# Performance work log

Hardware: AMD Instinct MI355X
Metric: run time of the kernel (lower is better)

## Reference

```python
import jax, jax.numpy as jnp
import numpy as np

# NTU RGB+D 25-joint skeleton edges (1-based)
NTU_EDGES = [(1,2),(2,21),(3,21),(4,3),(5,21),(6,5),(7,6),(8,7),(9,21),(10,9),
             (11,10),(12,11),(13,1),(14,13),(15,14),(16,15),(17,1),(18,17),
             (19,18),(20,19),(22,23),(23,8),(24,25),(25,12)]
NUM_SCALES = 13
NUM_POINT = 25


def build_A_powers(num_scales=NUM_SCALES, v=NUM_POINT):
    # MS-G3D disentangled multi-scale aggregation: exact-k-hop adjacencies, each
    # with self loops, symmetrically normalized, stacked along dim 0 -> (K*V, V).
    A = np.zeros((v, v))
    for i, j in NTU_EDGES:
        A[i - 1, j - 1] = 1.0
        A[j - 1, i - 1] = 1.0
    I = np.eye(v)
    mats = []
    for k in range(num_scales):
        if k == 0:
            Ak = I.copy()
        else:
            Ak = np.minimum(np.linalg.matrix_power(A + I, k), 1) \
               - np.minimum(np.linalg.matrix_power(A + I, k - 1), 1)
            Ak = Ak + I  # with_self=True
        d = Ak.sum(-1)
        dinv = np.where(d > 0, d ** -0.5, 0.0)
        mats.append((dinv[:, None] * Ak) * dinv[None, :])
    return np.concatenate(mats, 0).astype(np.float32)


def batchnorm(x, g, b, axes, ch_axis, eps=1e-5):
    # torch BatchNorm in training mode: biased batch stats + affine
    mean = jnp.mean(x, axes, keepdims=True)
    var = jnp.mean((x - mean) ** 2, axes, keepdims=True)
    shape = [1] * x.ndim
    shape[ch_axis] = -1
    return (x - mean) * jax.lax.rsqrt(var + eps) * g.reshape(shape) + b.reshape(shape)


def ms_gcn(x, A_powers, A_res, W, b, g, beta, num_scales):
    # x: (N, C, T, V); A: (K*V, V)
    A = A_powers + A_res
    support = jnp.einsum('vu,nctu->nctv', A, x)            # (N, C, T, K*V)
    N, C, T, KV = support.shape
    V = KV // num_scales
    support = support.reshape(N, C, T, num_scales, V).transpose(0, 3, 1, 2, 4)
    support = support.reshape(N, num_scales * C, T, V)     # (N, K*C, T, V)
    out = jnp.einsum('oc,nctv->notv', W, support) + b[None, :, None, None]  # 1x1 conv
    out = batchnorm(out, g, beta, (0, 2, 3), 1)
    return jax.nn.relu(out)


def lstm(x, Wih, Whh, bih, bhh):
    # single-layer batch_first LSTM, zero initial state; torch gate order i,f,g,o
    B = x.shape[0]
    H = Whh.shape[1]
    xp = jnp.einsum('bsd,hd->bsh', x, Wih) + bih + bhh     # precompute input proj

    def step(carry, xt):
        h, c = carry
        gates = xt + h @ Whh.T
        i, f, g, o = jnp.split(gates, 4, axis=-1)
        c = jax.nn.sigmoid(f) * c + jax.nn.sigmoid(i) * jnp.tanh(g)
        h = jax.nn.sigmoid(o) * jnp.tanh(c)
        return (h, c), h

    init = (jnp.zeros((B, H), x.dtype), jnp.zeros((B, H), x.dtype))
    _, ys = jax.lax.scan(step, init, jnp.swapaxes(xp, 0, 1))
    return jnp.swapaxes(ys, 0, 1)                          # (B, S, H)


def logsig_rnn(x, n_segments, Wih, Whh, bih, bhh):
    # x: (B, T, d). Depth-2 log-signature per time segment + segment start point,
    # concatenated and fed to an LSTM (Logsig-RNN layer).
    B, T, d = x.shape
    t_vec = np.array([int(round(float(v))) for v in np.linspace(1, T, n_segments + 1)])
    starts = t_vec[:-1] - 1
    ends = t_vec[1:] - 1
    L = int((ends - starts).max()) + 1
    # pad segments to fixed length by repeating the last point (zero increments)
    idx = np.minimum(starts[:, None] + np.arange(L)[None, :], ends[:, None])  # (S, L)
    pts = x[:, idx, :]                                     # (B, S, L, d)
    rel = pts - pts[:, :, :1, :]
    inc = rel[:, :, -1, :]                                 # level-1: total increment
    dx = pts[:, :, 1:, :] - pts[:, :, :-1, :]
    Mm = jnp.einsum('bsli,bslj->bsij', rel[:, :, :-1, :], dx)
    iu, ju = np.triu_indices(d, k=1)
    levy = 0.5 * (Mm[:, :, iu, ju] - Mm[:, :, ju, iu])     # level-2 (Lyndon basis)
    feats = jnp.concatenate([x[:, starts, :], inc, levy], axis=-1)
    return lstm(feats, Wih, Whh, bih, bhh)


def setup_inputs() -> dict:
    key = jax.random.key(0)
    ks = iter(jax.random.split(key, 16))
    N, C, T, V, M = 2, 3, 100, 25, 2
    c1, c2, num_class, K = 96, 192, 60, NUM_SCALES

    def randn(shape, scale):
        return jax.random.normal(next(ks), shape, jnp.float32) * scale

    ls1 = c1 + c1 * (c1 - 1) // 2     # 4656
    ls2 = c2 + c2 * (c2 - 1) // 2     # 18528
    in1 = c1 + ls1                    # 4752
    in2 = c2 + ls2                    # 18720
    Ap = jnp.asarray(build_A_powers())
    return {
        'x': jax.random.normal(next(ks), (N, C, T, V, M), jnp.float32),
        'length': jax.random.randint(next(ks), (N,), 0, T),
        'data_bn_g': jnp.ones((M * V * C,)), 'data_bn_b': jnp.zeros((M * V * C,)),
        'A_powers1': Ap,
        'A_res1': jax.random.uniform(next(ks), Ap.shape, jnp.float32, -1e-6, 1e-6),
        'W1': randn((c1, K * C), (K * C) ** -0.5), 'b1': jnp.zeros((c1,)),
        'bn1_g': jnp.ones((c1,)), 'bn1_b': jnp.zeros((c1,)),
        'Wih1': randn((4 * c1, in1), in1 ** -0.5), 'Whh1': randn((4 * c1, c1), c1 ** -0.5),
        'bih1': jnp.zeros((4 * c1,)), 'bhh1': jnp.zeros((4 * c1,)),
        'bnseg1_g': jnp.ones((50,)), 'bnseg1_b': jnp.zeros((50,)),
        'A_powers2': Ap,
        'A_res2': jax.random.uniform(next(ks), Ap.shape, jnp.float32, -1e-6, 1e-6),
        'W2': randn((c2, K * c1), (K * c1) ** -0.5), 'b2': jnp.zeros((c2,)),
        'bn2_g': jnp.ones((c2,)), 'bn2_b': jnp.zeros((c2,)),
        'Wih2': randn((4 * c2, in2), in2 ** -0.5), 'Whh2': randn((4 * c2, c2), c2 ** -0.5),
        'bih2': jnp.zeros((4 * c2,)), 'bhh2': jnp.zeros((4 * c2,)),
        'bnseg2_g': jnp.ones((30,)), 'bnseg2_b': jnp.zeros((30,)),
        'fcW': randn((num_class, c2), c2 ** -0.5), 'fcb': jnp.zeros((num_class,)),
    }


def reference(x, length, data_bn_g, data_bn_b, A_powers1, A_res1, W1, b1, bn1_g, bn1_b,
              Wih1, Whh1, bih1, bhh1, bnseg1_g, bnseg1_b, A_powers2, A_res2, W2, b2,
              bn2_g, bn2_b, Wih2, Whh2, bih2, bhh2, bnseg2_g, bnseg2_b, fcW, fcb):
    # `length` is accepted but unused, as in the original forward.
    N, C, T, V, M = x.shape
    K = A_powers1.shape[0] // V
    c1, c2 = W1.shape[0], W2.shape[0]
    S1, S2 = 50, 30

    h = x.transpose(0, 4, 3, 1, 2).reshape(N, M * V * C, T)
    h = batchnorm(h, data_bn_g, data_bn_b, (0, 2), 1)
    h = h.reshape(N * M, V, C, T).transpose(0, 2, 3, 1)            # (NM, C, T, V)

    h = jax.nn.relu(ms_gcn(h, A_powers1, A_res1, W1, b1, bn1_g, bn1_b, K))
    h = h.transpose(0, 3, 2, 1).reshape(N * M * V, T, c1)
    h = logsig_rnn(h, S1, Wih1, Whh1, bih1, bhh1)                  # (NMV, S1, c1)
    h = batchnorm(h, bnseg1_g, bnseg1_b, (0, 2), 1)
    h = h.reshape(N * M, V, S1, c1).transpose(0, 3, 2, 1)          # (NM, c1, S1, V)

    h = jax.nn.relu(ms_gcn(h, A_powers2, A_res2, W2, b2, bn2_g, bn2_b, K))
    h = h.transpose(0, 3, 2, 1).reshape(N * M * V, S1, c2)
    h = logsig_rnn(h, S2, Wih2, Whh2, bih2, bhh2)                  # (NMV, S2, c2)
    h = batchnorm(h, bnseg2_g, bnseg2_b, (0, 2), 1)
    h = h.reshape(N * M, V, S2, c2).transpose(0, 3, 2, 1)          # (NM, c2, S2, V)

    pooled = h.reshape(N, M, c2, -1).mean(axis=3).mean(axis=1)     # (N, c2)
    return pooled @ fcW.T + fcb
```

## Files before the change

### kernel.cpp

```cpp
#include <hip/hip_runtime.h>
#include <cmath>
#include <cstdint>
#include <cstddef>

typedef unsigned short bf16_t;
typedef __attribute__((ext_vector_type(8))) short short8;
typedef __attribute__((ext_vector_type(4))) float floatx4;
typedef __attribute__((ext_vector_type(2))) _Float16 half2_t;

__device__ __forceinline__ float bf2f(bf16_t b){
  unsigned int u = ((unsigned int)b) << 16;
  return __uint_as_float(u);
}
__device__ __forceinline__ bf16_t f2bf(float f){
  unsigned int u = __float_as_uint(f);
  unsigned int r = (u + 0x7fffu + ((u >> 16) & 1u)) >> 16;
  return (bf16_t)r;
}
__device__ __forceinline__ unsigned int f2bf2(float a, float b){
  return (unsigned int)f2bf(a) | ((unsigned int)f2bf(b) << 16);
}
__device__ __forceinline__ float sigf(float x){ return 1.0f / (1.0f + expf(-x)); }

__device__ __forceinline__ float dot2(half2_t a, half2_t b, float c){
#if __has_builtin(__builtin_amdgcn_fdot2)
  return __builtin_amdgcn_fdot2(a, b, c, false);
#else
  return c + (float)a.x * (float)b.x + (float)a.y * (float)b.y;
#endif
}

__device__ __forceinline__ void gload_lds16(const bf16_t* g, bf16_t* lds){
  __builtin_amdgcn_global_load_lds(
      (const __attribute__((address_space(1))) unsigned int*)g,
      (__attribute__((address_space(3))) unsigned int*)lds, 16, 0, 0);
}

__global__ void prep_misc(const float* __restrict__ a1, const float* __restrict__ r1, float* __restrict__ o1,
                          const float* __restrict__ a2, const float* __restrict__ r2, float* __restrict__ o2,
                          const float* __restrict__ bi1, const float* __restrict__ bh1, float* __restrict__ ob1,
                          const float* __restrict__ bi2, const float* __restrict__ bh2, float* __restrict__ ob2,
                          const float* __restrict__ Whh1, half2_t* __restrict__ Wp1,
                          const float* __restrict__ Whh2, half2_t* __restrict__ Wp2,
                          unsigned short* __restrict__ lut1, unsigned short* __restrict__ lut2,
                          float* __restrict__ stats, bf16_t* __restrict__ A2mat){
  int i = blockIdx.x * blockDim.x + threadIdx.x;
  if (i < 8125){ o1[i] = a1[i] + r1[i]; o2[i] = a2[i] + r2[i]; }
  if (i < 384) ob1[i] = bi1[i] + bh1[i];
  if (i < 768) ob2[i] = bi2[i] + bh2[i];
  if (i < 736) stats[i] = 0.f;
  if (i < 18432){
    int t = i % 384, j2 = i / 384;
    half2_t w; w.x = (_Float16)Whh1[(size_t)t * 96 + 2 * j2];
    w.y = (_Float16)Whh1[(size_t)t * 96 + 2 * j2 + 1];
    Wp1[i] = w;
  }
  if (i < 73728){
    int t = i % 768, j2 = i / 768;
    half2_t w; w.x = (_Float16)Whh2[(size_t)t * 192 + 2 * j2];
    w.y = (_Float16)Whh2[(size_t)t * 192 + 2 * j2 + 1];
    Wp2[i] = w;
  }
  if (i < 4560){
    int d = 96, p = i;
    int r = (int)(((2.0 * d - 1.0) - sqrt((2.0 * d - 1.0) * (2.0 * d - 1.0) - 8.0 * (double)p)) * 0.5);
    if (r < 0) r = 0;
    while (r + 1 <= d - 2 && (r + 1) * (d - 1) - ((r + 1) * r) / 2 <= p) ++r;
    while (r > 0 && r * (d - 1) - (r * (r - 1)) / 2 > p) --r;
    int jj = p - (r * (d - 1) - (r * (r - 1)) / 2);
    lut1[p] = (unsigned short)((r << 8) | (r + 1 + jj));
  }
  if (i < 18336){
    int d = 192, p = i;
    int r = (int)(((2.0 * d - 1.0) - sqrt((2.0 * d - 1.0) * (2.0 * d - 1.0) - 8.0 * (double)p)) * 0.5);
    if (r < 0) r = 0;
    while (r + 1 <= d - 2 && (r + 1) * (d - 1) - ((r + 1) * r) / 2 <= p) ++r;
    while (r > 0 && r * (d - 1) - (r * (r - 1)) / 2 > p) --r;
    int jj = p - (r * (d - 1) - (r * (r - 1)) / 2);
    lut2[p] = (unsigned short)((r << 8) | (r + 1 + jj));
  }
  if (i < 160000){
    int row = i >> 5, col = 1248 + (i & 31);
    A2mat[(size_t)row * 1280 + col] = 0;
  }
}

__global__ void f2bf_pad8(const float* __restrict__ in, bf16_t* __restrict__ out,
                          int R, int Kin, int Kout){
  int idx = blockIdx.x * blockDim.x + threadIdx.x;
  int ko8 = Kout >> 3;
  if (idx >= R * ko8) return;
  int r = idx / ko8, k8 = (idx % ko8) << 3;
  uint4 u;
  if (k8 + 8 <= Kin){
    const float4* p = reinterpret_cast<const float4*>(in + (size_t)r * Kin + k8);
    float4 x0 = p[0], x1 = p[1];
    u.x = f2bf2(x0.x, x0.y); u.y = f2bf2(x0.z, x0.w);
    u.z = f2bf2(x1.x, x1.y); u.w = f2bf2(x1.z, x1.w);
  } else {
    u.x = u.y = u.z = u.w = 0u;
  }
  *reinterpret_cast<uint4*>(out + (size_t)r * Kout + k8) = u;
}

__global__ void data_bn_kernel(const float* __restrict__ x, const float* __restrict__ g,
                               const float* __restrict__ bb, float* __restrict__ h1,
                               int N, int C, int T, int V, int M){
  int ch = blockIdx.x;
  int m = ch / (V * C);
  int v = (ch / C) % V;
  int c = ch % C;
  int tid = threadIdx.x;
  int cnt = N * T;
  float s = 0.f, s2 = 0.f;
  for (int i = tid; i < cnt; i += 64){
    int n = i / T, t = i % T;
    float val = x[(((size_t)(n * C + c) * T + t) * V + v) * M + m];
    s += val; s2 += val * val;
  }
  for (int off = 32; off; off >>= 1){ s += __shfl_down(s, off); s2 += __shfl_down(s2, off); }
  s = __shfl(s, 0); s2 = __shfl(s2, 0);
  float mean = s / cnt;
  float rstd = rsqrtf(s2 / cnt - mean * mean + 1e-5f);
  float gg = g[ch], bo = bb[ch];
  for (int i = tid; i < cnt; i += 64){
    int n = i / T, t = i % T;
    float val = x[(((size_t)(n * C + c) * T + t) * V + v) * M + m];
    float y = (val - mean) * rstd * gg + bo;
    h1[((size_t)((n * M + m) * C + c) * T + t) * V + v] = y;
  }
}

__global__ void support1_kernel(const float* __restrict__ A, const float* __restrict__ hin,
                                float* __restrict__ sup, int total){
  int idx = blockIdx.x * blockDim.x + threadIdx.x;
  if (idx >= total) return;
  int w = idx % 325;
  int rest = idx / 325;
  const float* row = hin + (size_t)rest * 25;
  const float* ar = A + w * 25;
  float acc = 0.f;
  #pragma unroll
  for (int u = 0; u < 25; ++u) acc += ar[u] * row[u];
  sup[idx] = acc;
}

__global__ void gcn1_out_kernel(const float* __restrict__ sup, const float* __restrict__ W1,
                                const float* __restrict__ b1, float* __restrict__ y1, int NM, int T){
  int idx = blockIdx.x * blockDim.x + threadIdx.x;
  int total = NM * T * 25 * 96;
  if (idx >= total) return;
  int o = idx % 96;
  int v = (idx / 96) % 25;
  int t = (idx / (96 * 25)) % T;
  int nm = idx / (96 * 25 * T);
  float acc = b1[o];
  #pragma unroll
  for (int k = 0; k < 13; ++k)
    #pragma unroll
    for (int c = 0; c < 3; ++c)
      acc += W1[o * 39 + k * 3 + c] * sup[(size_t)((nm * 3 + c) * T + t) * 325 + k * 25 + v];
  y1[idx] = acc;
}

__global__ void colstats_atomic(const float* __restrict__ mat, int R,
                                float* __restrict__ sum, float* __restrict__ sumsq){
  int col = threadIdx.x;
  int Cc = blockDim.x;
  float s = 0.f, s2 = 0.f;
  for (int r = blockIdx.x; r < R; r += gridDim.x){
    float v = mat[(size_t)r * Cc + col];
    s += v; s2 += v * v;
  }
  atomicAdd(&sum[col], s);
  atomicAdd(&sumsq[col], s2);
}

__global__ void segstats_atomic(const float* __restrict__ lout, int R2, int S,
                                float* __restrict__ sum, float* __restrict__ sumsq){
  int t = threadIdx.x;
  int H = blockDim.x;
  int nw = H >> 6;
  __shared__ float ra[4], rb[4];
  int lane = t & 63, wid = t >> 6;
  for (int r = blockIdx.x; r < R2; r += gridDim.x){
    int s = r % S;
    float v = lout[(size_t)r * H + t];
    float a = v, b2 = v * v;
    for (int off = 32; off; off >>= 1){ a += __shfl_down(a, off); b2 += __shfl_down(b2, off); }
    if (lane == 0){ ra[wid] = a; rb[wid] = b2; }
    __syncthreads();
    if (t == 0){
      float sa = 0.f, sb = 0.f;
      for (int w = 0; w < nw; ++w){ sa += ra[w]; sb += rb[w]; }
      atomicAdd(&sum[s], sa);
      atomicAdd(&sumsq[s], sb);
    }
    __syncthreads();
  }
}

__global__ void bn_relu_seq_kernel(const float* __restrict__ ymat, const float* __restrict__ sum,
                                   const float* __restrict__ sumsq, const float* __restrict__ g,
                                   const float* __restrict__ bb, float* __restrict__ xseq,
                                   int NM, int T, int H, int R){
  int idx = blockIdx.x * blockDim.x + threadIdx.x;
  int total = NM * T * 25 * H;
  if (idx >= total) return;
  int o = idx % H;
  int v = (idx / H) % 25;
  int t = (idx / (H * 25)) % T;
  int nm = idx / (H * 25 * T);
  float mean = sum[o] / R;
  float rstd = rsqrtf(sumsq[o] / R - mean * mean + 1e-5f);
  float val = (ymat[idx] - mean) * rstd * g[o] + bb[o];
  val = fmaxf(val, 0.f);
  int b = nm * 25 + v;
  xseq[((size_t)b * T + t) * H + o] = val;
}

struct SegTable { int st[50]; int en[50]; };

__global__ void feats_kernel(const float* __restrict__ xseq, bf16_t* __restrict__ feats,
                             SegTable segs, const unsigned short* __restrict__ lut,
                             int T, int d, int S, int L, int pairs, int rowlenP){
  __shared__ float pts[4][192];
  int bs = blockIdx.x;
  int b = bs / S, s = bs % S;
  int st = segs.st[s], en = segs.en[s];
  int nt = blockDim.x, tid = threadIdx.x;
  for (int l = 0; l < L; ++l){
    int t = st + l; if (t > en) t = en;
    for (int i = tid; i < d; i += nt) pts[l][i] = xseq[((size_t)b * T + t) * d + i];
  }
  __syncthreads();
  int rowlen = 2 * d + pairs;
  bf16_t* frow = feats + (size_t)bs * rowlenP;
  for (int i = tid; i < d; i += nt){
    frow[i] = f2bf(pts[0][i]);
    frow[d + i] = f2bf(pts[L - 1][i] - pts[0][i]);
  }
  for (int i = tid + rowlen; i < rowlenP; i += nt) frow[i] = 0;
  int Lm2 = L - 2;
  bf16_t* lrow = frow + 2 * d;
  for (int p = tid; p < pairs; p += nt){
    int e = lut[p];
    int i = e >> 8, j = e & 255;
    float acc = 0.f;
    for (int l = 1; l <= Lm2; ++l){
      float ri = pts[l][i] - pts[0][i], rj = pts[l][j] - pts[0][j];
      float di = pts[l + 1][i] - pts[l][i], dj = pts[l + 1][j] - pts[l][j];
      acc += ri * dj - rj * di;
    }
    lrow[p] = f2bf(0.5f * acc);
  }
}

__global__ __launch_bounds__(256)
void gemm_mfma_nt_split(const bf16_t* __restrict__ A, const bf16_t* __restrict__ B,
                        float* __restrict__ P, int M, int N, int K){
  __shared__ bf16_t As[128 * 64];
  __shared__ bf16_t Bs[128 * 64];
  const int tid = threadIdx.x;
  const int lane = tid & 63, wv = tid >> 6;
  const int bm = blockIdx.x * 128, bn = blockIdx.y * 128;
  const int wr = (wv >> 1) * 64, wc = (wv & 1) * 64;
  const int m_l = lane & 15, q = lane >> 4;

  const int ksteps = K >> 6;
  const int Z = gridDim.z, z = blockIdx.z;
  const int per = (ksteps + Z - 1) / Z;
  const int ks0 = z * per;
  const int ks1 = (ks0 + per < ksteps) ? ks0 + per : ksteps;

  const int rlane = lane >> 3;
  const int slane = lane & 7;
  const int colc = (slane ^ rlane) * 8;
  const bf16_t* gA[4]; const bf16_t* gB[4];
  bf16_t* lA[4]; bf16_t* lB[4];
  #pragma unroll
  for (int it = 0; it < 4; ++it){
    int c = it * 4 + wv;
    int rowA = bm + c * 8 + rlane; if (rowA > M - 1) rowA = M - 1;
    int rowB = bn + c * 8 + rlane; if (rowB > N - 1) rowB = N - 1;
    gA[it] = A + (size_t)rowA * K + colc;
    gB[it] = B + (size_t)rowB * K + colc;
    lA[it] = &As[c * 512];
    lB[it] = &Bs[c * 512];
  }
  const int sxor = m_l & 7;

  floatx4 acc[4][4] = {};
  for (int ks = ks0; ks < ks1; ++ks){
    int k0 = ks << 6;
    __syncthreads();
    #pragma unroll
    for (int it = 0; it < 4; ++it){
      gload_lds16(gA[it] + k0, lA[it]);
      gload_lds16(gB[it] + k0, lB[it]);
    }
    __syncthreads();
    #pragma unroll
    for (int half = 0; half < 2; ++half){
      const int scol = ((half * 4 + q) ^ sxor) * 8;
      short8 af[4], bfr[4];
      #pragma unroll
      for (int i = 0; i < 4; ++i){
        af[i]  = *reinterpret_cast<const short8*>(&As[(wr + i * 16 + m_l) * 64 + scol]);
        bfr[i] = *reinterpret_cast<const short8*>(&Bs[(wc + i * 16 + m_l) * 64 + scol]);
      }
      #pragma unroll
      for (int mi = 0; mi < 4; ++mi)
        #pragma unroll
        for (int ni = 0; ni < 4; ++ni)
          acc[mi][ni] = __builtin_amdgcn_mfma_f32_16x16x32_bf16(af[mi], bfr[ni], acc[mi][ni], 0, 0, 0);
    }
  }

  float* Pz = P + (size_t)z * M * N;
  #pragma unroll
  for (int mi = 0; mi < 4; ++mi){
    int row0 = bm + wr + mi * 16 + q * 4;
    #pragma unroll
    for (int r = 0; r < 4; ++r){
      int row = row0 + r;
      if (row < M){
        #pragma unroll
        for (int ni = 0; ni < 4; ++ni){
          int col = bn + wc + ni * 16 + m_l;
          if (col < N) Pz[(size_t)row * N + col] = acc[mi][ni][r];
        }
      }
    }
  }
}

__global__ void reduce_split_bias(const float* __restrict__ P, const float* __restrict__ bias,
                                  float* __restrict__ out, int MN, int N, int Z){
  int i4 = (blockIdx.x * blockDim.x + threadIdx.x) * 4;
  if (i4 >= MN) return;
  const float4 bv = *reinterpret_cast<const float4*>(bias + (i4 % N));
  float4 s = bv;
  for (int z = 0; z < Z; ++z){
    const float4 p = *reinterpret_cast<const float4*>(P + (size_t)z * MN + i4);
    s.x += p.x; s.y += p.y; s.z += p.z; s.w += p.w;
  }
  *reinterpret_cast<float4*>(out + i4) = s;
}

template <int H2C, int BLK, int Z>
__global__ __launch_bounds__(BLK)
void lstm_kernel(const float* __restrict__ P, const float* __restrict__ bias,
                 const half2_t* __restrict__ Wp, float* __restrict__ out,
                 int S, int MN){
  constexpr int H = 2 * H2C;
  constexpr int H4 = 4 * H;
  __shared__ _Float16 __attribute__((aligned(16))) hsh[H];
  __shared__ float gv[H4];
  const int b = blockIdx.x, t = threadIdx.x;
  half2_t w[H2C];
  const half2_t* wp = Wp + t;
  #pragma unroll
  for (int j2 = 0; j2 < H2C; ++j2) w[j2] = wp[(size_t)j2 * H4];
  float cc = 0.f;
  if (t < H) hsh[t] = (_Float16)0.f;
  const float bval = bias[t];
  __syncthreads();
  const half2_t* hp = reinterpret_cast<const half2_t*>(hsh);
  for (int s = 0; s < S; ++s){
    size_t rowoff = ((size_t)b * S + s) * H4 + t;
    float pv[Z];
    #pragma unroll
    for (int z = 0; z < Z; ++z) pv[z] = P[(size_t)z * MN + rowoff];
    float a0 = bval, a1 = 0.f, a2 = 0.f, a3 = 0.f;
    #pragma unroll
    for (int z = 0; z < Z; ++z) a0 += pv[z];
    #pragma unroll
    for (int j2 = 0; j2 < H2C; j2 += 4){
      a0 = dot2(w[j2],     hp[j2],     a0);
      a1 = dot2(w[j2 + 1], hp[j2 + 1], a1);
      a2 = dot2(w[j2 + 2], hp[j2 + 2], a2);
      a3 = dot2(w[j2 + 3], hp[j2 + 3], a3);
    }
    gv[t] = (a0 + a1) + (a2 + a3);
    __syncthreads();
    if (t < H){
      float ig = sigf(gv[t]);
      float fg = sigf(gv[H + t]);
      float gg = tanhf(gv[2 * H + t]);
      float og = sigf(gv[3 * H + t]);
      cc = fg * cc + ig * gg;
      float hh = og * tanhf(cc);
      hsh[t] = (_Float16)hh;
      out[((size_t)b * S + s) * H + t] = hh;
    }
    __syncthreads();
  }
}

__global__ void bnseg_to_g2in_kernel(const float* __restrict__ lout, const float* __restrict__ sum,
                                     const float* __restrict__ sumsq, const float* __restrict__ g,
                                     const float* __restrict__ bb, float* __restrict__ g2in,
                                     int B, int S, int H, int cnt){
  int idx = blockIdx.x * blockDim.x + threadIdx.x;
  int total = B * S * H;
  if (idx >= total) return;
  int hh = idx % H;
  int s = (idx / H) % S;
  int b = idx / (H * S);
  float mean = sum[s] / cnt;
  float rstd = rsqrtf(sumsq[s] / cnt - mean * mean + 1e-5f);
  float val = (lout[idx] - mean) * rstd * g[s] + bb[s];
  int nm = b / 25, v = b % 25;
  g2in[((size_t)((nm * H + hh) * S) + s) * 25 + v] = val;
}

__global__ void support2_kernel(const float* __restrict__ A, const float* __restrict__ g2in,
                                bf16_t* __restrict__ A2mat, int NM, int C1, int S){
  int idx = blockIdx.x * blockDim.x + threadIdx.x;
  int total = NM * C1 * S * 325;
  if (idx >= total) return;
  int w = idx % 325;
  int s = (idx / 325) % S;
  int c = (idx / (325 * S)) % C1;
  int nm = idx / (325 * S * C1);
  const float* row = g2in + ((size_t)((nm * C1 + c) * S) + s) * 25;
  const float* ar = A + w * 25;
  float acc = 0.f;
  #pragma unroll
  for (int u = 0; u < 25; ++u) acc += ar[u] * row[u];
  int k = w / 25, v = w % 25;
  A2mat[((size_t)((nm * S + s) * 25 + v)) * 1280 + k * C1 + c] = f2bf(acc);
}

__global__ void pool_kernel(const float* __restrict__ lout2, const float* __restrict__ sum,
                            const float* __restrict__ sumsq, const float* __restrict__ g,
                            const float* __restrict__ bb, float* __restrict__ pooled,
                            int S, int H, int scnt){
  int n = blockIdx.x / H;
  int o = blockIdx.x % H;
  float acc = 0.f;
  int cnt = 2 * 25 * S;
  for (int i = threadIdx.x; i < cnt; i += 64){
    int m = i / (25 * S);
    int r = i % (25 * S);
    int v = r / S;
    int s = r % S;
    int b = (n * 2 + m) * 25 + v;
    float val = lout2[((size_t)b * S + s) * H + o];
    float mean = sum[s] / scnt;
    float rstd = rsqrtf(sumsq[s] / scnt - mean * mean + 1e-5f);
    val = (val - mean) * rstd * g[s] + bb[s];
    acc += val;
  }
  for (int off = 32; off; off >>= 1) acc += __shfl_down(acc, off);
  if (threadIdx.x == 0) pooled[n * H + o] = acc / cnt;
}

__global__ void fc_kernel(const float* __restrict__ pooled, const float* __restrict__ fcW,
                          const float* __restrict__ fcb, float* __restrict__ outp){
  int idx = blockIdx.x * blockDim.x + threadIdx.x;
  if (idx >= 120) return;
  int n = idx / 60, cls = idx % 60;
  float acc = fcb[cls];
  for (int o = 0; o < 192; ++o) acc += pooled[n * 192 + o] * fcW[cls * 192 + o];
  outp[idx] = acc;
}

static void make_segs(int T, int S, SegTable& tab, int& L){
  double step = (double)(T - 1) / (double)S;
  long long tv[51];
  for (int i = 0; i <= S; ++i){
    double v = 1.0 + step * (double)i;
    tv[i] = llrint(v);
  }
  L = 0;
  for (int s = 0; s < S; ++s){
    tab.st[s] = (int)tv[s] - 1;
    tab.en[s] = (int)tv[s + 1] - 1;
    int len = tab.en[s] - tab.st[s] + 1;
    if (len > L) L = len;
  }
  for (int s = S; s < 50; ++s){ tab.st[s] = 0; tab.en[s] = 0; }
  if (L > 4) L = 4;
}

extern "C" void kernel_launch(void* const* d_in, const int* in_sizes, int n_in,
                              void* d_out, int out_size, void* d_ws, size_t ws_size,
                              hipStream_t stream){
  const float* x         = (const float*)d_in[0];
  const float* data_bn_g = (const float*)d_in[2];
  const float* data_bn_b = (const float*)d_in[3];
  const float* A_powers1 = (const float*)d_in[4];
  const float* A_res1    = (const float*)d_in[5];
  const float* W1        = (const float*)d_in[6];
  const float* b1        = (const float*)d_in[7];
  const float* bn1_g     = (const float*)d_in[8];
  const float* bn1_b     = (const float*)d_in[9];
  const float* Wih1      = (const float*)d_in[10];
  const float* Whh1      = (const float*)d_in[11];
  const float* bih1      = (const float*)d_in[12];
  const float* bhh1      = (const float*)d_in[13];
  const float* bnseg1_g  = (const float*)d_in[14];
  const float* bnseg1_b  = (const float*)d_in[15];
  const float* A_powers2 = (const float*)d_in[16];
  const float* A_res2    = (const float*)d_in[17];
  const float* W2        = (const float*)d_in[18];
  const float* b2        = (const float*)d_in[19];
  const float* bn2_g     = (const float*)d_in[20];
  const float* bn2_b     = (const float*)d_in[21];
  const float* Wih2      = (const float*)d_in[22];
  const float* Whh2      = (const float*)d_in[23];
  const float* bih2      = (const float*)d_in[24];
  const float* bhh2      = (const float*)d_in[25];
  const float* bnseg2_g  = (const float*)d_in[26];
  const float* bnseg2_b  = (const float*)d_in[27];
  const float* fcW       = (const float*)d_in[28];
  const float* fcb       = (const float*)d_in[29];
  float* out = (float*)d_out;

  const int N = 2, C = 3, T = 100, V = 25, M = 2, NM = 4;
  const int K = 13, C1 = 96, C2 = 192;
  const int S1 = 50, S2 = 30;
  const int B = 100;
  const int IN1 = 4752, IN2 = 18720;
  const int IN1P = 4800, IN2P = 18752;
  const int P1 = 4560, P2 = 18336;
  const int KG2 = 1248, KG2P = 1280;
  const int Z1 = 5, Z2 = 6, ZG = 4;

  size_t off = 0;
  char* base = (char*)d_ws;
  auto alloc = [&](size_t nbytes) -> void* {
    off = (off + 255) & ~(size_t)255;
    void* p = base + off;
    off += nbytes;
    return p;
  };
  float* A1full = (float*)alloc(325 * 25 * 4);
  float* A2full = (float*)alloc(325 * 25 * 4);
  float* h1     = (float*)alloc((size_t)NM * C * T * V * 4);
  float* sup1   = (float*)alloc((size_t)NM * C * T * 325 * 4);
  float* y1mat  = (float*)alloc((size_t)NM * T * V * C1 * 4);
  float* stats  = (float*)alloc(736 * 4);
  float* st1a = stats, *st1b = stats + 96;
  float* sg1a = stats + 192, *sg1b = stats + 242;
  float* st2a = stats + 292, *st2b = stats + 484;
  float* sg2a = stats + 676, *sg2b = stats + 706;
  float* xseq1  = (float*)alloc((size_t)B * T * C1 * 4);
  float* l1out  = (float*)alloc((size_t)B * S1 * C1 * 4);
  float* g2in   = (float*)alloc((size_t)NM * C1 * S1 * V * 4);
  bf16_t* A2mat = (bf16_t*)alloc((size_t)NM * S1 * V * KG2P * 2);
  float* y2mat  = (float*)alloc((size_t)NM * S1 * V * C2 * 4);
  float* xseq2  = (float*)alloc((size_t)B * S1 * C2 * 4);
  float* l2out  = (float*)alloc((size_t)B * S2 * C2 * 4);
  float* pooled = (float*)alloc(2 * C2 * 4);
  float* bias1  = (float*)alloc(4 * C1 * 4);
  float* bias2  = (float*)alloc(4 * C2 * 4);
  half2_t* Wp1  = (half2_t*)alloc((size_t)(C1 / 2) * 4 * C1 * 4);
  half2_t* Wp2  = (half2_t*)alloc((size_t)(C2 / 2) * 4 * C2 * 4);
  bf16_t* Wih1b = (bf16_t*)alloc((size_t)4 * C1 * IN1P * 2);
  bf16_t* Wih2b = (bf16_t*)alloc((size_t)4 * C2 * IN2P * 2);
  bf16_t* W2b   = (bf16_t*)alloc((size_t)C2 * KG2P * 2);
  unsigned short* lut1 = (unsigned short*)alloc((size_t)P1 * 2);
  unsigned short* lut2 = (unsigned short*)alloc((size_t)P2 * 2);
  size_t pmax = (size_t)Z2 * 3000 * 768;
  {
    size_t p1s = (size_t)Z1 * 5000 * 384; if (p1s > pmax) pmax = p1s;
    size_t pgs = (size_t)ZG * 5000 * 192; if (pgs > pmax) pmax = pgs;
  }
  float* Pbuf = (float*)alloc(pmax * 4);
  bf16_t* feats = (bf16_t*)alloc((size_t)B * S2 * IN2P * 2);
  (void)ws_size; (void)in_sizes; (void)n_in; (void)out_size;

  prep_misc<<<625, 256, 0, stream>>>(A_powers1, A_res1, A1full, A_powers2, A_res2, A2full,
                                     bih1, bhh1, bias1, bih2, bhh2, bias2,
                                     Whh1, Wp1, Whh2, Wp2, lut1, lut2, stats, A2mat);
  f2bf_pad8<<<(4 * C1 * (IN1P / 8) + 255) / 256, 256, 0, stream>>>(Wih1, Wih1b, 4 * C1, IN1, IN1P);
  f2bf_pad8<<<(4 * C2 * (IN2P / 8) + 255) / 256, 256, 0, stream>>>(Wih2, Wih2b, 4 * C2, IN2, IN2P);
  f2bf_pad8<<<(C2 * (KG2P / 8) + 255) / 256, 256, 0, stream>>>(W2, W2b, C2, KG2, KG2P);

  data_bn_kernel<<<M * V * C, 64, 0, stream>>>(x, data_bn_g, data_bn_b, h1, N, C, T, V, M);

  int tot_sup1 = NM * C * T * 325;
  support1_kernel<<<(tot_sup1 + 255) / 256, 256, 0, stream>>>(A1full, h1, sup1, tot_sup1);
  int tot_y1 = NM * T * 25 * C1;
  gcn1_out_kernel<<<(tot_y1 + 255) / 256, 256, 0, stream>>>(sup1, W1, b1, y1mat, NM, T);
  colstats_atomic<<<256, C1, 0, stream>>>(y1mat, NM * T * 25, st1a, st1b);
  bn_relu_seq_kernel<<<(tot_y1 + 255) / 256, 256, 0, stream>>>(y1mat, st1a, st1b, bn1_g, bn1_b,
                                                               xseq1, NM, T, C1, NM * T * 25);

  SegTable seg1, seg2; int L1, L2;
  make_segs(T, S1, seg1, L1);
  make_segs(S1, S2, seg2, L2);

  feats_kernel<<<B * S1, 256, 0, stream>>>(xseq1, feats, seg1, lut1, T, C1, S1, L1, P1, IN1P);
  {
    int Mm = B * S1, Nn = 4 * C1;
    dim3 g((Mm + 127) / 128, (Nn + 127) / 128, Z1);
    gemm_mfma_nt_split<<<g, 256, 0, stream>>>(feats, Wih1b, Pbuf, Mm, Nn, IN1P);
    lstm_kernel<48, 384, Z1><<<B, 384, 0, stream>>>(Pbuf, bias1, Wp1, l1out, S1, Mm * Nn);
  }
  segstats_atomic<<<256, C1, 0, stream>>>(l1out, B * S1, S1, sg1a, sg1b);
  int tot_bn1 = B * S1 * C1;
  bnseg_to_g2in_kernel<<<(tot_bn1 + 255) / 256, 256, 0, stream>>>(l1out, sg1a, sg1b, bnseg1_g,
                                                                  bnseg1_b, g2in, B, S1, C1, B * C1);

  int tot_sup2 = NM * C1 * S1 * 325;
  support2_kernel<<<(tot_sup2 + 255) / 256, 256, 0, stream>>>(A2full, g2in, A2mat, NM, C1, S1);
  {
    int Mm = NM * S1 * 25, Nn = C2;
    dim3 g((Mm + 127) / 128, (Nn + 127) / 128, ZG);
    gemm_mfma_nt_split<<<g, 256, 0, stream>>>(A2mat, W2b, Pbuf, Mm, Nn, KG2P);
    int MN = Mm * Nn;
    reduce_split_bias<<<(MN / 4 + 255) / 256, 256, 0, stream>>>(Pbuf, b2, y2mat, MN, Nn, ZG);
  }
  colstats_atomic<<<256, C2, 0, stream>>>(y2mat, NM * S1 * 25, st2a, st2b);
  int tot_y2 = NM * S1 * 25 * C2;
  bn_relu_seq_kernel<<<(tot_y2 + 255) / 256, 256, 0, stream>>>(y2mat, st2a, st2b, bn2_g, bn2_b,
                                                               xseq2, NM, S1, C2, NM * S1 * 25);

  feats_kernel<<<B * S2, 256, 0, stream>>>(xseq2, feats, seg2, lut2, S1, C2, S2, L2, P2, IN2P);
  {
    int Mm = B * S2, Nn = 4 * C2;
    dim3 g((Mm + 127) / 128, (Nn + 127) / 128, Z2);
    gemm_mfma_nt_split<<<g, 256, 0, stream>>>(feats, Wih2b, Pbuf, Mm, Nn, IN2P);
    lstm_kernel<96, 768, Z2><<<B, 768, 0, stream>>>(Pbuf, bias2, Wp2, l2out, S2, Mm * Nn);
  }
  segstats_atomic<<<256, C2, 0, stream>>>(l2out, B * S2, S2, sg2a, sg2b);

  pool_kernel<<<2 * C2, 64, 0, stream>>>(l2out, sg2a, sg2b, bnseg2_g, bnseg2_b, pooled, S2, C2, B * C2);
  fc_kernel<<<1, 128, 0, stream>>>(pooled, fcW, fcb, out);
}
```

Before: 764.2 us.

## Merge weight conversions, pack feature writes, prefetch LSTM inputs, reorder g2in layout

The three weight bf16-conversion launches become one merged kernel. feats_kernel now handles two log-signature pairs per thread with 32-bit packed LUT reads and bf16x2 stores. The LSTM kernel prefetches the precomputed input projections two steps ahead and uses eight dot2 accumulators instead of four. The g2in intermediate changes to channel-innermost layout so support2 reads and writes coalesce along channels. The changes aim to cut launch overhead, narrow stores, global-load latency on the serial LSTM path and uncoalesced accesses, at the cost of more registers and hardcoded sizes (96, 13).

```diff
diff --git a/kernel.cpp b/kernel.cpp
--- a/kernel.cpp
+++ b/kernel.cpp
@@ -85,12 +85,9 @@
   }
 }
 
-__global__ void f2bf_pad8(const float* __restrict__ in, bf16_t* __restrict__ out,
-                          int R, int Kin, int Kout){
-  int idx = blockIdx.x * blockDim.x + threadIdx.x;
+__device__ __forceinline__ void f2bf_seg(const float* in, bf16_t* out, int Kin, int Kout, int li){
   int ko8 = Kout >> 3;
-  if (idx >= R * ko8) return;
-  int r = idx / ko8, k8 = (idx % ko8) << 3;
+  int r = li / ko8, k8 = (li % ko8) << 3;
   uint4 u;
   if (k8 + 8 <= Kin){
     const float4* p = reinterpret_cast<const float4*>(in + (size_t)r * Kin + k8);
@@ -101,6 +98,17 @@
     u.x = u.y = u.z = u.w = 0u;
   }
   *reinterpret_cast<uint4*>(out + (size_t)r * Kout + k8) = u;
+}
+
+__global__ void f2bf_pad8_3(const float* __restrict__ in1, bf16_t* __restrict__ out1, int Kin1, int Kout1, int c1,
+                            const float* __restrict__ in2, bf16_t* __restrict__ out2, int Kin2, int Kout2, int c2,
+                            const float* __restrict__ in3, bf16_t* __restrict__ out3, int Kin3, int Kout3, int c3){
+  int idx = blockIdx.x * blockDim.x + threadIdx.x;
+  if (idx < c1){ f2bf_seg(in1, out1, Kin1, Kout1, idx); return; }
+  idx -= c1;
+  if (idx < c2){ f2bf_seg(in2, out2, Kin2, Kout2, idx); return; }
+  idx -= c2;
+  if (idx < c3) f2bf_seg(in3, out3, Kin3, Kout3, idx);
 }
 
 __global__ void data_bn_kernel(const float* __restrict__ x, const float* __restrict__ g,
@@ -222,7 +230,7 @@
 struct SegTable { int st[50]; int en[50]; };
 
 __global__ void feats_kernel(const float* __restrict__ xseq, bf16_t* __restrict__ feats,
-                             SegTable segs, const unsigned short* __restrict__ lut,
+                             SegTable segs, const unsigned int* __restrict__ lut32,
                              int T, int d, int S, int L, int pairs, int rowlenP){
   __shared__ float pts[4][192];
   int bs = blockIdx.x;
@@ -234,25 +242,33 @@
     for (int i = tid; i < d; i += nt) pts[l][i] = xseq[((size_t)b * T + t) * d + i];
   }
   __syncthreads();
-  int rowlen = 2 * d + pairs;
-  bf16_t* frow = feats + (size_t)bs * rowlenP;
-  for (int i = tid; i < d; i += nt){
-    frow[i] = f2bf(pts[0][i]);
-    frow[d + i] = f2bf(pts[L - 1][i] - pts[0][i]);
-  }
-  for (int i = tid + rowlen; i < rowlenP; i += nt) frow[i] = 0;
+  unsigned int* frow32 = reinterpret_cast<unsigned int*>(feats + (size_t)bs * rowlenP);
+  int d2 = d >> 1;
+  for (int i2 = tid; i2 < d2; i2 += nt){
+    int i = 2 * i2;
+    frow32[i2]      = f2bf2(pts[0][i], pts[0][i + 1]);
+    frow32[d2 + i2] = f2bf2(pts[L - 1][i] - pts[0][i], pts[L - 1][i + 1] - pts[0][i + 1]);
+  }
+  int rowlen2 = (2 * d + pairs) >> 1, rowlenP2 = rowlenP >> 1;
+  for (int i = tid + rowlen2; i < rowlenP2; i += nt) frow32[i] = 0;
   int Lm2 = L - 2;
-  bf16_t* lrow = frow + 2 * d;
-  for (int p = tid; p < pairs; p += nt){
-    int e = lut[p];
-    int i = e >> 8, j = e & 255;
-    float acc = 0.f;
+  unsigned int* lrow32 = frow32 + d;
+  int pairs2 = pairs >> 1;
+  for (int p2 = tid; p2 < pairs2; p2 += nt){
+    unsigned int ee = lut32[p2];
+    int i0 = (ee >> 8) & 255, j0 = ee & 255;
+    int i1 = ee >> 24, j1 = (ee >> 16) & 255;
+    float acc0 = 0.f, acc1 = 0.f;
     for (int l = 1; l <= Lm2; ++l){
-      float ri = pts[l][i] - pts[0][i], rj = pts[l][j] - pts[0][j];
-      float di = pts[l + 1][i] - pts[l][i], dj = pts[l + 1][j] - pts[l][j];
-      acc += ri * dj - rj * di;
-    }
-    lrow[p] = f2bf(0.5f * acc);
+      float p0i = pts[0][i0], p0j = pts[0][j0], p0i1 = pts[0][i1], p0j1 = pts[0][j1];
+      float ri = pts[l][i0] - p0i, rj = pts[l][j0] - p0j;
+      float di = pts[l + 1][i0] - pts[l][i0], dj = pts[l + 1][j0] - pts[l][j0];
+      acc0 += ri * dj - rj * di;
+      float ri1 = pts[l][i1] - p0i1, rj1 = pts[l][j1] - p0j1;
+      float di1 = pts[l + 1][i1] - pts[l][i1], dj1 = pts[l + 1][j1] - pts[l][j1];
+      acc1 += ri1 * dj1 - rj1 * di1;
+    }
+    lrow32[p2] = f2bf2(0.5f * acc0, 0.5f * acc1);
   }
 }
 
@@ -365,24 +381,37 @@
   float cc = 0.f;
   if (t < H) hsh[t] = (_Float16)0.f;
   const float bval = bias[t];
+  const size_t base = (size_t)b * S * H4 + t;
+  float pv0[Z], pv1[Z];
+  #pragma unroll
+  for (int z = 0; z < Z; ++z) pv0[z] = P[(size_t)z * MN + base];
+  #pragma unroll
+  for (int z = 0; z < Z; ++z) pv1[z] = P[(size_t)z * MN + base + H4];
   __syncthreads();
   const half2_t* hp = reinterpret_cast<const half2_t*>(hsh);
   for (int s = 0; s < S; ++s){
-    size_t rowoff = ((size_t)b * S + s) * H4 + t;
-    float pv[Z];
+    float pvn[Z];
+    if (s + 2 < S){
+      size_t o2 = base + (size_t)(s + 2) * H4;
+      #pragma unroll
+      for (int z = 0; z < Z; ++z) pvn[z] = P[(size_t)z * MN + o2];
+    }
+    float a0 = bval, a1 = 0.f, a2 = 0.f, a3 = 0.f;
+    float a4 = 0.f, a5 = 0.f, a6 = 0.f, a7 = 0.f;
     #pragma unroll
-    for (int z = 0; z < Z; ++z) pv[z] = P[(size_t)z * MN + rowoff];
-    float a0 = bval, a1 = 0.f, a2 = 0.f, a3 = 0.f;
+    for (int z = 0; z < Z; ++z) a0 += pv0[z];
     #pragma unroll
-    for (int z = 0; z < Z; ++z) a0 += pv[z];
-    #pragma unroll
-    for (int j2 = 0; j2 < H2C; j2 += 4){
+    for (int j2 = 0; j2 < H2C; j2 += 8){
       a0 = dot2(w[j2],     hp[j2],     a0);
       a1 = dot2(w[j2 + 1], hp[j2 + 1], a1);
       a2 = dot2(w[j2 + 2], hp[j2 + 2], a2);
       a3 = dot2(w[j2 + 3], hp[j2 + 3], a3);
-    }
-    gv[t] = (a0 + a1) + (a2 + a3);
+      a4 = dot2(w[j2 + 4], hp[j2 + 4], a4);
+      a5 = dot2(w[j2 + 5], hp[j2 + 5], a5);
+      a6 = dot2(w[j2 + 6], hp[j2 + 6], a6);
+      a7 = dot2(w[j2 + 7], hp[j2 + 7], a7);
+    }
+    gv[t] = ((a0 + a1) + (a2 + a3)) + ((a4 + a5) + (a6 + a7));
     __syncthreads();
     if (t < H){
       float ig = sigf(gv[t]);
@@ -395,6 +424,8 @@
       out[((size_t)b * S + s) * H + t] = hh;
     }
     __syncthreads();
+    #pragma unroll
+    for (int z = 0; z < Z; ++z){ pv0[z] = pv1[z]; pv1[z] = pvn[z]; }
   }
 }
 
@@ -412,25 +443,24 @@
   float rstd = rsqrtf(sumsq[s] / cnt - mean * mean + 1e-5f);
   float val = (lout[idx] - mean) * rstd * g[s] + bb[s];
   int nm = b / 25, v = b % 25;
-  g2in[((size_t)((nm * H + hh) * S) + s) * 25 + v] = val;
+  g2in[(((size_t)(nm * S + s) * 25 + v) * H) + hh] = val;
 }
 
 __global__ void support2_kernel(const float* __restrict__ A, const float* __restrict__ g2in,
                                 bf16_t* __restrict__ A2mat, int NM, int C1, int S){
   int idx = blockIdx.x * blockDim.x + threadIdx.x;
-  int total = NM * C1 * S * 325;
+  int total = NM * S * 25 * 13 * 96;
   if (idx >= total) return;
-  int w = idx % 325;
-  int s = (idx / 325) % S;
-  int c = (idx / (325 * S)) % C1;
-  int nm = idx / (325 * S * C1);
-  const float* row = g2in + ((size_t)((nm * C1 + c) * S) + s) * 25;
-  const float* ar = A + w * 25;
+  int c = idx % 96;
+  int k = (idx / 96) % 13;
+  int v = (idx / (96 * 13)) % 25;
+  int rs = idx / (96 * 13 * 25);
+  const float* gbase = g2in + ((size_t)rs * 25) * 96 + c;
+  const float* ar = A + (k * 25 + v) * 25;
   float acc = 0.f;
   #pragma unroll
-  for (int u = 0; u < 25; ++u) acc += ar[u] * row[u];
-  int k = w / 25, v = w % 25;
-  A2mat[((size_t)((nm * S + s) * 25 + v)) * 1280 + k * C1 + c] = f2bf(acc);
+  for (int u = 0; u < 25; ++u) acc += ar[u] * gbase[(size_t)u * 96];
+  A2mat[((size_t)rs * 25 + v) * 1280 + k * 96 + c] = f2bf(acc);
 }
 
 __global__ void pool_kernel(const float* __restrict__ lout2, const float* __restrict__ sum,
@@ -549,7 +579,7 @@
   float* sg2a = stats + 676, *sg2b = stats + 706;
   float* xseq1  = (float*)alloc((size_t)B * T * C1 * 4);
   float* l1out  = (float*)alloc((size_t)B * S1 * C1 * 4);
-  float* g2in   = (float*)alloc((size_t)NM * C1 * S1 * V * 4);
+  float* g2in   = (float*)alloc((size_t)NM * S1 * V * C1 * 4);
   bf16_t* A2mat = (bf16_t*)alloc((size_t)NM * S1 * V * KG2P * 2);
   float* y2mat  = (float*)alloc((size_t)NM * S1 * V * C2 * 4);
   float* xseq2  = (float*)alloc((size_t)B * S1 * C2 * 4);
@@ -576,9 +606,15 @@
   prep_misc<<<625, 256, 0, stream>>>(A_powers1, A_res1, A1full, A_powers2, A_res2, A2full,
                                      bih1, bhh1, bias1, bih2, bhh2, bias2,
                                      Whh1, Wp1, Whh2, Wp2, lut1, lut2, stats, A2mat);
-  f2bf_pad8<<<(4 * C1 * (IN1P / 8) + 255) / 256, 256, 0, stream>>>(Wih1, Wih1b, 4 * C1, IN1, IN1P);
-  f2bf_pad8<<<(4 * C2 * (IN2P / 8) + 255) / 256, 256, 0, stream>>>(Wih2, Wih2b, 4 * C2, IN2, IN2P);
-  f2bf_pad8<<<(C2 * (KG2P / 8) + 255) / 256, 256, 0, stream>>>(W2, W2b, C2, KG2, KG2P);
+  {
+    int c1 = 4 * C1 * (IN1P / 8);
+    int c2 = 4 * C2 * (IN2P / 8);
+    int c3 = C2 * (KG2P / 8);
+    int tot = c1 + c2 + c3;
+    f2bf_pad8_3<<<(tot + 255) / 256, 256, 0, stream>>>(Wih1, Wih1b, IN1, IN1P, c1,
+                                                       Wih2, Wih2b, IN2, IN2P, c2,
+                                                       W2, W2b, KG2, KG2P, c3);
+  }
 
   data_bn_kernel<<<M * V * C, 64, 0, stream>>>(x, data_bn_g, data_bn_b, h1, N, C, T, V, M);
 
@@ -594,7 +630,8 @@
   make_segs(T, S1, seg1, L1);
   make_segs(S1, S2, seg2, L2);
 
-  feats_kernel<<<B * S1, 256, 0, stream>>>(xseq1, feats, seg1, lut1, T, C1, S1, L1, P1, IN1P);
+  feats_kernel<<<B * S1, 256, 0, stream>>>(xseq1, feats, seg1, (const unsigned int*)lut1,
+                                           T, C1, S1, L1, P1, IN1P);
   {
     int Mm = B * S1, Nn = 4 * C1;
     dim3 g((Mm + 127) / 128, (Nn + 127) / 128, Z1);
@@ -606,7 +643,7 @@
   bnseg_to_g2in_kernel<<<(tot_bn1 + 255) / 256, 256, 0, stream>>>(l1out, sg1a, sg1b, bnseg1_g,
                                                                   bnseg1_b, g2in, B, S1, C1, B * C1);
 
-  int tot_sup2 = NM * C1 * S1 * 325;
+  int tot_sup2 = NM * S1 * 25 * 13 * 96;
   support2_kernel<<<(tot_sup2 + 255) / 256, 256, 0, stream>>>(A2full, g2in, A2mat, NM, C1, S1);
   {
     int Mm = NM * S1 * 25, Nn = C2;
@@ -620,7 +657,8 @@
   bn_relu_seq_kernel<<<(tot_y2 + 255) / 256, 256, 0, stream>>>(y2mat, st2a, st2b, bn2_g, bn2_b,
                                                                xseq2, NM, S1, C2, NM * S1 * 25);
 
-  feats_kernel<<<B * S2, 256, 0, stream>>>(xseq2, feats, seg2, lut2, S1, C2, S2, L2, P2, IN2P);
+  feats_kernel<<<B * S2, 256, 0, stream>>>(xseq2, feats, seg2, (const unsigned int*)lut2,
+                                           S1, C2, S2, L2, P2, IN2P);
   {
     int Mm = B * S2, Nn = 4 * C2;
     dim3 g((Mm + 127) / 128, (Nn + 127) / 128, Z2);
```

Result: faster. 706.7 us (-7.5%).
